# Optimization experiments

Hardware: AMD Instinct MI355X
Metric: run time of the kernel (lower is better)

The kernel has to match this reference:

```python
import jax, jax.numpy as jnp
import numpy as np

TEMPERATURE = 1.0
EPS = 1e-12


def _l2_normalize(x, axis):
    # torch F.normalize: x / max(||x||_2, eps)
    n = jnp.sqrt(jnp.sum(x * x, axis=axis, keepdims=True))
    return x / jnp.maximum(n, EPS)


def setup_inputs() -> dict:
    key = jax.random.key(0)
    k1, k2 = jax.random.split(key)
    B, C, H, W = 2, 128, 128, 256
    K = 20
    features = jax.random.normal(k1, (B, C, H, W), dtype=jnp.float32)
    prototypes = jax.random.normal(k2, (K, C), dtype=jnp.float32)
    distance_scale = jnp.ones((1,), dtype=jnp.float32)
    return {"features": features, "prototypes": prototypes, "distance_scale": distance_scale}


def reference(features, prototypes, distance_scale):
    # features: [B, C, H, W] -> transpose(1,3) -> [B, W, H, C]
    f = jnp.transpose(features, (0, 3, 2, 1))
    # torch F.normalize default dim=1: on [B, W, H, C] this is the W axis (faithful)
    fn = _l2_normalize(f, axis=1)
    # prototypes [K, C], normalized along dim=1 (features)
    pn = _l2_normalize(prototypes, axis=1)
    # exact euclidean cdist (donot_use_mm): broadcasted diff [B, W, H, K, C]
    diff = fn[:, :, :, None, :] - pn[None, None, None, :, :]
    dist = jnp.sqrt(jnp.sum(diff * diff, axis=-1))  # [B, W, H, K]
    dist = jnp.abs(distance_scale) * dist
    # transpose(3,1): [B, K, H, W]
    logits = -jnp.transpose(dist, (0, 3, 2, 1))
    return logits / TEMPERATURE
```

## Files before the change

kernel.cpp:

```cpp
#include <hip/hip_runtime.h>
#include <math.h>

#define B 2
#define C 128
#define H 128
#define W 256
#define K 20
#define HW (H * W)

__global__ __launch_bounds__(256) void isomax_prep(
    const float* __restrict__ feats, const float* __restrict__ protos,
    float* __restrict__ rn_ws, float* __restrict__ pn_ws, float* __restrict__ ppsum_ws)
{
    const int tid = threadIdx.x, wave = tid >> 6, lane = tid & 63;
    const int blk = blockIdx.x;

    if (blk < 8192) {
        const int r = blk * 4 + wave;
        const float4 v = ((const float4*)(feats + (size_t)r * W))[lane];
        float ss = fmaf(v.x, v.x, fmaf(v.y, v.y, fmaf(v.z, v.z, v.w * v.w)));
        #pragma unroll
        for (int off = 32; off > 0; off >>= 1) ss += __shfl_xor(ss, off, 64);
        if (lane == 0) {
            const int h  = r & (H - 1);
            const int bc = r >> 7;
            const int c  = bc & (C - 1);
            const int b  = bc >> 7;
            rn_ws[(b * H + h) * C + c] = 1.0f / fmaxf(sqrtf(ss), 1e-12f);
        }
    } else {
        __shared__ float s_rp[32];
        __shared__ float s_pp[32];
        for (int k = wave; k < K; k += 4) {
            const float* p = protos + k * C;
            float a = p[lane], bq = p[lane + 64];
            float ss = fmaf(a, a, bq * bq);
            #pragma unroll
            for (int off = 32; off > 0; off >>= 1) ss += __shfl_xor(ss, off, 64);
            if (lane == 0) {
                float n  = sqrtf(ss);
                float rp = 1.0f / fmaxf(n, 1e-12f);
                s_rp[k] = rp;
                float nn = n * rp;
                s_pp[k] = nn * nn;
            }
        }
        __syncthreads();
        for (int i = tid; i < C * K; i += 256) {
            const int kg  = i / 640;
            const int rem = i - kg * 640;
            const int c   = rem / 5;
            const int j   = rem - c * 5;
            const int k   = kg * 5 + j;
            pn_ws[i] = protos[k * C + c] * s_rp[k];
        }
        if (tid < K) ppsum_ws[tid] = s_pp[tid];
    }
}

__global__ __launch_bounds__(256, 4) void isomax_dist(
    const float* __restrict__ feats, const float* __restrict__ rn_ws,
    const float* __restrict__ pn_ws, const float* __restrict__ ppsum_ws,
    const float* __restrict__ dscale, float* __restrict__ out)
{
    const int tid = threadIdx.x;
    const int kg  = __builtin_amdgcn_readfirstlane(tid >> 6);
    const int wl  = tid & 63;
    const int blk = blockIdx.x;
    const int wt  = blk & 3;
    const int bh  = blk >> 2;
    const int b   = bh >> 7;
    const int h   = bh & 127;
    const int w   = wt * 64 + wl;

    const float* fp = feats + ((size_t)b * C * H + h) * W + w;
    const float* rn = rn_ws + bh * C;
    const float* pk = pn_ws + kg * (C * 5);

    float S = 0.f;
    float dacc[5] = {0.f, 0.f, 0.f, 0.f, 0.f};

    #pragma unroll 4
    for (int c0 = 0; c0 < C; c0 += 4) {
        const float4 r4 = *(const float4*)(rn + c0);
        float pp[20];
        ((float4*)pp)[0] = *(const float4*)(pk + c0 * 5 + 0);
        ((float4*)pp)[1] = *(const float4*)(pk + c0 * 5 + 4);
        ((float4*)pp)[2] = *(const float4*)(pk + c0 * 5 + 8);
        ((float4*)pp)[3] = *(const float4*)(pk + c0 * 5 + 12);
        ((float4*)pp)[4] = *(const float4*)(pk + c0 * 5 + 16);

        const float v0 = fp[(size_t)(c0 + 0) * HW] * r4.x;
        const float v1 = fp[(size_t)(c0 + 1) * HW] * r4.y;
        const float v2 = fp[(size_t)(c0 + 2) * HW] * r4.z;
        const float v3 = fp[(size_t)(c0 + 3) * HW] * r4.w;
        S = fmaf(v0, v0, S);
        S = fmaf(v1, v1, S);
        S = fmaf(v2, v2, S);
        S = fmaf(v3, v3, S);
        #pragma unroll
        for (int j = 0; j < 5; ++j) {
            float d = dacc[j];
            d = fmaf(v0, pp[j],      d);
            d = fmaf(v1, pp[5 + j],  d);
            d = fmaf(v2, pp[10 + j], d);
            d = fmaf(v3, pp[15 + j], d);
            dacc[j] = d;
        }
    }

    const float scale = fabsf(dscale[0]);
    const float* pps = ppsum_ws + kg * 5;
    float* ob = out + ((size_t)b * K * H + h) * W + w;
    #pragma unroll
    for (int j = 0; j < 5; ++j) {
        const int k = kg * 5 + j;
        float dist2 = fmaxf(fmaf(-2.f, dacc[j], S + pps[j]), 0.f);
        ob[(size_t)k * HW] = -scale * sqrtf(dist2);
    }
}

extern "C" void kernel_launch(void* const* d_in, const int* in_sizes, int n_in,
                              void* d_out, int out_size, void* d_ws, size_t ws_size,
                              hipStream_t stream) {
    const float* feats  = (const float*)d_in[0];
    const float* protos = (const float*)d_in[1];
    const float* dscale = (const float*)d_in[2];
    float* out = (float*)d_out;

    float* rn_ws    = (float*)d_ws;
    float* pn_ws    = rn_ws + 32768;
    float* ppsum_ws = pn_ws + 2560;

    isomax_prep<<<8193, 256, 0, stream>>>(feats, protos, rn_ws, pn_ws, ppsum_ws);
    isomax_dist<<<B * H * (W / 64), 256, 0, stream>>>(feats, rn_ws, pn_ws, ppsum_ws,
                                                      dscale, out);
}
```

Measured before the change: 96.91 us.

## Stage per-row scaled prototypes in LDS and process two columns per thread

The distance kernel now builds a per-(b,h) table in shared memory that folds the -2·rn[c] scaling into the prototype values and stores rn²·, so the inner loop is pure FMAs. Each thread handles two adjacent w positions with float2 loads and stores. This halves the grid and reuses each prototype value across two columns. The per-block table build adds a prologue and a barrier, and the prep kernel's prototype layout becomes plain row-major. Fewer blocks (512) may reduce latency hiding.

```diff
diff --git a/kernel.cpp b/kernel.cpp
--- a/kernel.cpp
+++ b/kernel.cpp
@@ -47,76 +47,81 @@
         }
         __syncthreads();
         for (int i = tid; i < C * K; i += 256) {
-            const int kg  = i / 640;
-            const int rem = i - kg * 640;
-            const int c   = rem / 5;
-            const int j   = rem - c * 5;
-            const int k   = kg * 5 + j;
-            pn_ws[i] = protos[k * C + c] * s_rp[k];
+            const int k = i >> 7;
+            pn_ws[i] = protos[i] * s_rp[k];
         }
         if (tid < K) ppsum_ws[tid] = s_pp[tid];
     }
 }
 
-__global__ __launch_bounds__(256, 4) void isomax_dist(
+__global__ __launch_bounds__(256) void isomax_dist(
     const float* __restrict__ feats, const float* __restrict__ rn_ws,
     const float* __restrict__ pn_ws, const float* __restrict__ ppsum_ws,
     const float* __restrict__ dscale, float* __restrict__ out)
 {
-    const int tid = threadIdx.x;
-    const int kg  = __builtin_amdgcn_readfirstlane(tid >> 6);
-    const int wl  = tid & 63;
-    const int blk = blockIdx.x;
-    const int wt  = blk & 3;
-    const int bh  = blk >> 2;
-    const int b   = bh >> 7;
-    const int h   = bh & 127;
-    const int w   = wt * 64 + wl;
+    __shared__ __align__(16) float s_pd[C][4][8];
+    __shared__ float s_pp[K];
 
-    const float* fp = feats + ((size_t)b * C * H + h) * W + w;
+    const int tid   = threadIdx.x;
+    const int blk   = blockIdx.x;
+    const int whalf = blk & 1;
+    const int bh    = blk >> 1;
+    const int b     = bh >> 7;
+    const int h     = bh & 127;
+    const int kg    = tid >> 6;
+    const int lane  = tid & 63;
+
     const float* rn = rn_ws + bh * C;
-    const float* pk = pn_ws + kg * (C * 5);
 
-    float S = 0.f;
-    float dacc[5] = {0.f, 0.f, 0.f, 0.f, 0.f};
+    for (int i = tid; i < C * K; i += 256) {
+        const int c  = i / K;
+        const int k  = i - c * K;
+        const int g  = k / 5;
+        const int j  = k - g * 5;
+        s_pd[c][g][j] = -2.0f * rn[c] * pn_ws[k * C + c];
+    }
+    for (int i = tid; i < C * 4; i += 256) {
+        const int c = i >> 2, g = i & 3;
+        const float r = rn[c];
+        s_pd[c][g][5] = r * r;
+    }
+    if (tid < K) s_pp[tid] = ppsum_ws[tid];
+    __syncthreads();
 
-    #pragma unroll 4
-    for (int c0 = 0; c0 < C; c0 += 4) {
-        const float4 r4 = *(const float4*)(rn + c0);
-        float pp[20];
-        ((float4*)pp)[0] = *(const float4*)(pk + c0 * 5 + 0);
-        ((float4*)pp)[1] = *(const float4*)(pk + c0 * 5 + 4);
-        ((float4*)pp)[2] = *(const float4*)(pk + c0 * 5 + 8);
-        ((float4*)pp)[3] = *(const float4*)(pk + c0 * 5 + 12);
-        ((float4*)pp)[4] = *(const float4*)(pk + c0 * 5 + 16);
+    const int w0 = whalf * 128 + lane * 2;
+    const float* fp = feats + ((size_t)(b * C) * H + h) * W + w0;
 
-        const float v0 = fp[(size_t)(c0 + 0) * HW] * r4.x;
-        const float v1 = fp[(size_t)(c0 + 1) * HW] * r4.y;
-        const float v2 = fp[(size_t)(c0 + 2) * HW] * r4.z;
-        const float v3 = fp[(size_t)(c0 + 3) * HW] * r4.w;
-        S = fmaf(v0, v0, S);
-        S = fmaf(v1, v1, S);
-        S = fmaf(v2, v2, S);
-        S = fmaf(v3, v3, S);
-        #pragma unroll
-        for (int j = 0; j < 5; ++j) {
-            float d = dacc[j];
-            d = fmaf(v0, pp[j],      d);
-            d = fmaf(v1, pp[5 + j],  d);
-            d = fmaf(v2, pp[10 + j], d);
-            d = fmaf(v3, pp[15 + j], d);
-            dacc[j] = d;
-        }
+    float d0[5] = {0.f, 0.f, 0.f, 0.f, 0.f};
+    float d1[5] = {0.f, 0.f, 0.f, 0.f, 0.f};
+    float S0 = 0.f, S1 = 0.f;
+
+    #pragma unroll 8
+    for (int c = 0; c < C; ++c) {
+        const float2 f2 = *(const float2*)(fp + (size_t)c * HW);
+        const float* pd = s_pd[c][kg];
+        const float p0 = pd[0], p1 = pd[1], p2 = pd[2], p3 = pd[3];
+        const float p4 = pd[4], r2 = pd[5];
+        S0 = fmaf(f2.x * f2.x, r2, S0);
+        S1 = fmaf(f2.y * f2.y, r2, S1);
+        d0[0] = fmaf(f2.x, p0, d0[0]);  d1[0] = fmaf(f2.y, p0, d1[0]);
+        d0[1] = fmaf(f2.x, p1, d0[1]);  d1[1] = fmaf(f2.y, p1, d1[1]);
+        d0[2] = fmaf(f2.x, p2, d0[2]);  d1[2] = fmaf(f2.y, p2, d1[2]);
+        d0[3] = fmaf(f2.x, p3, d0[3]);  d1[3] = fmaf(f2.y, p3, d1[3]);
+        d0[4] = fmaf(f2.x, p4, d0[4]);  d1[4] = fmaf(f2.y, p4, d1[4]);
     }
 
     const float scale = fabsf(dscale[0]);
-    const float* pps = ppsum_ws + kg * 5;
-    float* ob = out + ((size_t)b * K * H + h) * W + w;
+    float* ob = out + ((size_t)(b * K) * H + h) * W + w0;
     #pragma unroll
     for (int j = 0; j < 5; ++j) {
         const int k = kg * 5 + j;
-        float dist2 = fmaxf(fmaf(-2.f, dacc[j], S + pps[j]), 0.f);
-        ob[(size_t)k * HW] = -scale * sqrtf(dist2);
+        const float pp = s_pp[k];
+        float q0 = fmaxf(S0 + pp + d0[j], 0.f);
+        float q1 = fmaxf(S1 + pp + d1[j], 0.f);
+        float2 o;
+        o.x = -scale * sqrtf(q0);
+        o.y = -scale * sqrtf(q1);
+        *(float2*)(ob + (size_t)k * HW) = o;
     }
 }
 
@@ -133,6 +138,6 @@
     float* ppsum_ws = pn_ws + 2560;
 
     isomax_prep<<<8193, 256, 0, stream>>>(feats, protos, rn_ws, pn_ws, ppsum_ws);
-    isomax_dist<<<B * H * (W / 64), 256, 0, stream>>>(feats, rn_ws, pn_ws, ppsum_ws,
-                                                      dscale, out);
+    isomax_dist<<<B * H * 2, 256, 0, stream>>>(feats, rn_ws, pn_ws, ppsum_ws,
+                                               dscale, out);
 }
```

After: 95.42 us. No clear change (-1.5%).

## Compute feature-prototype dot products with bf16 MFMA via LDS-staged tiles

Applied to the files above, without the earlier changes.

The distance kernel now stages the normalized feature tile in swizzled LDS and computes the dot products with bf16 16x16x32 MFMA instructions. Previously each thread ran scalar FP32 FMAs over five prototypes. The prep kernel packs the normalized prototypes into bf16 MFMA B-fragment layout, padded to 32, and computes their squared norms from the rounded bf16 values. Output is written through LDS as coalesced float4 stores. This cuts ALU work but adds bf16 rounding error to the dot products and extra LDS traffic and syncs.

```diff
diff --git a/kernel.cpp b/kernel.cpp
--- a/kernel.cpp
+++ b/kernel.cpp
@@ -8,9 +8,20 @@
 #define K 20
 #define HW (H * W)
 
+typedef float f32x4 __attribute__((ext_vector_type(4)));
+typedef short bf16x8 __attribute__((ext_vector_type(8)));
+
+__device__ __forceinline__ unsigned f2bf_bits(float x) {
+    unsigned u = __float_as_uint(x);
+    return (u + 0x7FFFu + ((u >> 16) & 1u)) >> 16;
+}
+__device__ __forceinline__ float bf_to_f(unsigned bits) {
+    return __uint_as_float(bits << 16);
+}
+
 __global__ __launch_bounds__(256) void isomax_prep(
     const float* __restrict__ feats, const float* __restrict__ protos,
-    float* __restrict__ rn_ws, float* __restrict__ pn_ws, float* __restrict__ ppsum_ws)
+    float* __restrict__ rn_ws, short* __restrict__ pnf_ws, float* __restrict__ ppsum_ws)
 {
     const int tid = threadIdx.x, wave = tid >> 6, lane = tid & 63;
     const int blk = blockIdx.x;
@@ -30,93 +41,126 @@
         }
     } else {
         __shared__ float s_rp[32];
-        __shared__ float s_pp[32];
         for (int k = wave; k < K; k += 4) {
             const float* p = protos + k * C;
             float a = p[lane], bq = p[lane + 64];
             float ss = fmaf(a, a, bq * bq);
             #pragma unroll
             for (int off = 32; off > 0; off >>= 1) ss += __shfl_xor(ss, off, 64);
-            if (lane == 0) {
-                float n  = sqrtf(ss);
-                float rp = 1.0f / fmaxf(n, 1e-12f);
-                s_rp[k] = rp;
-                float nn = n * rp;
-                s_pp[k] = nn * nn;
-            }
+            if (lane == 0) s_rp[k] = 1.0f / fmaxf(sqrtf(ss), 1e-12f);
         }
         __syncthreads();
-        for (int i = tid; i < C * K; i += 256) {
-            const int kg  = i / 640;
-            const int rem = i - kg * 640;
-            const int c   = rem / 5;
-            const int j   = rem - c * 5;
-            const int k   = kg * 5 + j;
-            pn_ws[i] = protos[k * C + c] * s_rp[k];
+        for (int i = tid; i < 4096; i += 256) {
+            const int j  = i & 7;
+            const int ln = (i >> 3) & 63;
+            const int ch = (i >> 9) & 3;
+            const int t  = i >> 11;
+            const int c  = ch * 32 + ((ln >> 4) & 3) * 8 + j;
+            const int k  = t * 16 + (ln & 15);
+            float val = (k < K) ? protos[k * C + c] * s_rp[k] : 0.0f;
+            pnf_ws[i] = (short)f2bf_bits(val);
         }
-        if (tid < K) ppsum_ws[tid] = s_pp[tid];
+        if (tid < 32) {
+            float s = 0.f;
+            if (tid < K) {
+                const float rp = s_rp[tid];
+                for (int c = 0; c < C; ++c) {
+                    float pb = bf_to_f(f2bf_bits(protos[tid * C + c] * rp));
+                    s = fmaf(pb, pb, s);
+                }
+            }
+            ppsum_ws[tid] = s;
+        }
     }
 }
 
 __global__ __launch_bounds__(256, 4) void isomax_dist(
     const float* __restrict__ feats, const float* __restrict__ rn_ws,
-    const float* __restrict__ pn_ws, const float* __restrict__ ppsum_ws,
+    const short* __restrict__ pnf_ws, const float* __restrict__ ppsum_ws,
     const float* __restrict__ dscale, float* __restrict__ out)
 {
-    const int tid = threadIdx.x;
-    const int kg  = __builtin_amdgcn_readfirstlane(tid >> 6);
-    const int wl  = tid & 63;
-    const int blk = blockIdx.x;
-    const int wt  = blk & 3;
-    const int bh  = blk >> 2;
-    const int b   = bh >> 7;
-    const int h   = bh & 127;
-    const int w   = wt * 64 + wl;
+    __shared__ float s_u[C * 68];
+    __shared__ float s_S[64];
 
-    const float* fp = feats + ((size_t)b * C * H + h) * W + w;
-    const float* rn = rn_ws + bh * C;
-    const float* pk = pn_ws + kg * (C * 5);
+    const int tid  = threadIdx.x;
+    const int wave = tid >> 6, lane = tid & 63;
+    const int quad = lane >> 4, l16 = lane & 15;
+    const int blk  = blockIdx.x;
+    const int wq   = blk & 3;
+    const int bh   = blk >> 2;
+    const int b    = bh >> 7, h = bh & 127;
+    const int w0   = wq * 64;
 
-    float S = 0.f;
-    float dacc[5] = {0.f, 0.f, 0.f, 0.f, 0.f};
+    bf16x8 bfrag[4][2];
+    #pragma unroll
+    for (int t = 0; t < 2; ++t)
+        #pragma unroll
+        for (int ch = 0; ch < 4; ++ch)
+            bfrag[ch][t] = ((const bf16x8*)pnf_ws)[(t * 4 + ch) * 64 + lane];
+    const float pcol0 = ppsum_ws[l16];
+    const float pcol1 = ppsum_ws[16 + l16];
+    const float scale = fabsf(dscale[0]);
 
-    #pragma unroll 4
-    for (int c0 = 0; c0 < C; c0 += 4) {
-        const float4 r4 = *(const float4*)(rn + c0);
-        float pp[20];
-        ((float4*)pp)[0] = *(const float4*)(pk + c0 * 5 + 0);
-        ((float4*)pp)[1] = *(const float4*)(pk + c0 * 5 + 4);
-        ((float4*)pp)[2] = *(const float4*)(pk + c0 * 5 + 8);
-        ((float4*)pp)[3] = *(const float4*)(pk + c0 * 5 + 12);
-        ((float4*)pp)[4] = *(const float4*)(pk + c0 * 5 + 16);
-
-        const float v0 = fp[(size_t)(c0 + 0) * HW] * r4.x;
-        const float v1 = fp[(size_t)(c0 + 1) * HW] * r4.y;
-        const float v2 = fp[(size_t)(c0 + 2) * HW] * r4.z;
-        const float v3 = fp[(size_t)(c0 + 3) * HW] * r4.w;
-        S = fmaf(v0, v0, S);
-        S = fmaf(v1, v1, S);
-        S = fmaf(v2, v2, S);
-        S = fmaf(v3, v3, S);
+    {
+        const int wl = l16 * 4;
         #pragma unroll
-        for (int j = 0; j < 5; ++j) {
-            float d = dacc[j];
-            d = fmaf(v0, pp[j],      d);
-            d = fmaf(v1, pp[5 + j],  d);
-            d = fmaf(v2, pp[10 + j], d);
-            d = fmaf(v3, pp[15 + j], d);
-            dacc[j] = d;
+        for (int r = 0; r < 8; ++r) {
+            const int c  = wave * 32 + quad + r * 4;
+            const float rn = rn_ws[bh * C + c];
+            const float4 f4 = *(const float4*)(feats + ((size_t)(b * C + c) * H + h) * W + w0 + wl);
+            float4 u4;
+            u4.x = f4.x * rn; u4.y = f4.y * rn; u4.z = f4.z * rn; u4.w = f4.w * rn;
+            const int swz = ((c >> 3) & 1) << 4;
+            *(float4*)&s_u[c * 68 + (wl ^ swz)] = u4;
         }
     }
+    __syncthreads();
 
-    const float scale = fabsf(dscale[0]);
-    const float* pps = ppsum_ws + kg * 5;
-    float* ob = out + ((size_t)b * K * H + h) * W + w;
+    f32x4 acc0 = {0.f, 0.f, 0.f, 0.f}, acc1 = {0.f, 0.f, 0.f, 0.f};
+    float Sp = 0.f;
+    const int wm = wave * 16 + l16;
+    const int rswz = (quad & 1) << 4;
     #pragma unroll
-    for (int j = 0; j < 5; ++j) {
-        const int k = kg * 5 + j;
-        float dist2 = fmaxf(fmaf(-2.f, dacc[j], S + pps[j]), 0.f);
-        ob[(size_t)k * HW] = -scale * sqrtf(dist2);
+    for (int ch = 0; ch < 4; ++ch) {
+        float uj[8];
+        #pragma unroll
+        for (int j = 0; j < 8; ++j)
+            uj[j] = s_u[(ch * 32 + quad * 8 + j) * 68 + (wm ^ rswz)];
+        bf16x8 af;
+        #pragma unroll
+        for (int j = 0; j < 8; ++j) {
+            Sp = fmaf(uj[j], uj[j], Sp);
+            af[j] = (short)f2bf_bits(uj[j]);
+        }
+        acc0 = __builtin_amdgcn_mfma_f32_16x16x32_bf16(af, bfrag[ch][0], acc0, 0, 0, 0);
+        acc1 = __builtin_amdgcn_mfma_f32_16x16x32_bf16(af, bfrag[ch][1], acc1, 0, 0, 0);
+    }
+
+    Sp += __shfl_xor(Sp, 16, 64);
+    Sp += __shfl_xor(Sp, 32, 64);
+    if (lane < 16) s_S[wave * 16 + lane] = Sp;
+    __syncthreads();
+
+    const float4 sr4 = *(const float4*)&s_S[wave * 16 + quad * 4];
+    const float srv[4] = {sr4.x, sr4.y, sr4.z, sr4.w};
+
+    float* s_o = s_u;
+    #pragma unroll
+    for (int r = 0; r < 4; ++r) {
+        const int wl = wave * 16 + quad * 4 + r;
+        float d20 = srv[r] + pcol0 - 2.0f * acc0[r];
+        s_o[l16 * 68 + wl] = -scale * sqrtf(fmaxf(d20, 0.f));
+        if (l16 < 4) {
+            float d21 = srv[r] + pcol1 - 2.0f * acc1[r];
+            s_o[(16 + l16) * 68 + wl] = -scale * sqrtf(fmaxf(d21, 0.f));
+        }
+    }
+    __syncthreads();
+
+    for (int i = tid; i < K * 16; i += 256) {
+        const int k = i >> 4, g = i & 15;
+        const float4 v = *(const float4*)&s_o[k * 68 + g * 4];
+        *(float4*)(out + (size_t)(b * K + k) * HW + h * W + w0 + g * 4) = v;
     }
 }
 
@@ -129,10 +173,10 @@
     float* out = (float*)d_out;
 
     float* rn_ws    = (float*)d_ws;
-    float* pn_ws    = rn_ws + 32768;
-    float* ppsum_ws = pn_ws + 2560;
+    float* ppsum_ws = rn_ws + 32768;
+    short* pnf_ws   = (short*)(ppsum_ws + 32);
 
-    isomax_prep<<<8193, 256, 0, stream>>>(feats, protos, rn_ws, pn_ws, ppsum_ws);
-    isomax_dist<<<B * H * (W / 64), 256, 0, stream>>>(feats, rn_ws, pn_ws, ppsum_ws,
-                                                      dscale, out);
+    isomax_prep<<<8193, 256, 0, stream>>>(feats, protos, rn_ws, pnf_ws, ppsum_ws);
+    isomax_dist<<<B * H * 4, 256, 0, stream>>>(feats, rn_ws, pnf_ws, ppsum_ws,
+                                               dscale, out);
 }
```

Measured after the change: 91.53 us. -5.5%, faster.
